# Performance work log

Measured on AMD Instinct MI355X. Metric: run time of the kernel, lower is better.

Reference implementation:

```python
import jax, jax.numpy as jnp
import numpy as np

EMBED_DIM = 128
NUM_HEADS = 4
WIN = (7, 7)
N = WIN[0] * WIN[1]  # 49
NW = 64              # windows per image
B = 128              # batch of images
SCALE = (EMBED_DIM // NUM_HEADS) ** -0.5


def _relative_position_index():
    coords = np.stack(np.meshgrid(np.arange(WIN[0]), np.arange(WIN[1]), indexing='ij'))
    cf = coords.reshape(2, -1)                       # [2, N]
    rel = cf[:, :, None] - cf[:, None, :]            # [2, N, N]
    rel = rel.transpose(1, 2, 0).astype(np.int64)    # [N, N, 2]
    rel[..., 0] += WIN[0] - 1
    rel[..., 0] *= 2 * WIN[1] - 1
    rel[..., 1] += WIN[1] - 1
    return rel.sum(-1).reshape(-1)                   # [N*N]


def setup_inputs() -> dict:
    key = jax.random.key(0)
    ks = jax.random.split(key, 6)
    C = EMBED_DIM
    x = jax.random.normal(ks[0], (NW * B, N, C), dtype=jnp.float32)
    mask = jnp.zeros((NW, N, N), dtype=jnp.float32)
    qkv_w = jax.random.normal(ks[1], (3 * C, C), dtype=jnp.float32) * (C ** -0.5)
    qkv_b = jnp.zeros((3 * C,), dtype=jnp.float32)
    proj_w = jax.random.normal(ks[2], (C, C), dtype=jnp.float32) * (C ** -0.5)
    proj_b = jnp.zeros((C,), dtype=jnp.float32)
    bias_table = jax.random.normal(ks[3], ((2 * WIN[0] - 1) * (2 * WIN[1] - 1), NUM_HEADS), dtype=jnp.float32) * 0.02
    rel_index = jnp.asarray(_relative_position_index(), dtype=jnp.int32)
    return {"x": x, "mask": mask, "qkv_w": qkv_w, "qkv_b": qkv_b,
            "proj_w": proj_w, "proj_b": proj_b, "bias_table": bias_table,
            "rel_index": rel_index}


def reference(x, mask, qkv_w, qkv_b, proj_w, proj_b, bias_table, rel_index):
    nwb, n, c = x.shape
    nh, ch = NUM_HEADS, c // NUM_HEADS
    qkv = x @ qkv_w.T + qkv_b                               # [nwb, n, 3c]
    qkv = qkv.reshape(nwb, n, 3, nh, ch)
    q, k, v = (jnp.moveaxis(qkv, (2, 3), (0, 2))[i] for i in range(3))  # each [nwb, nh, n, ch]
    attn = jnp.einsum('whik,whjk->whij', q * SCALE, k)      # [nwb, nh, n, n]
    # relative position bias: gather then reshape to [1, nh, n, n]
    bias = bias_table[rel_index].reshape(n, n, nh).transpose(2, 0, 1)[None]
    attn = attn + bias
    if mask is not None:
        nw = mask.shape[0]
        attn = attn.reshape(nwb // nw, nw, nh, n, n) + mask[None, :, None]
        attn = attn.reshape(nwb, nh, n, n)
    attn = jax.nn.softmax(attn, axis=-1)
    out = jnp.einsum('whij,whjd->whid', attn, v)            # [nwb, nh, n, ch]
    out = out.transpose(0, 2, 1, 3).reshape(nwb, n, c)
    return out @ proj_w.T + proj_b
```

## Files before the change

kernel.cpp:

```cpp
#include <hip/hip_runtime.h>

typedef __bf16 bf16x8 __attribute__((ext_vector_type(8)));
typedef float  f32x4  __attribute__((ext_vector_type(4)));

#define NTOK  49
#define CDIM  128
#define QK_SCALE 0.17677669529663687f

#define XS 136
#define QS 264
#define VS 72
#define PS 64

#define WQKV_OFF  0
#define WPROJ_OFF 98304
#define BIASF_OFF 131072

__global__ void prep_kernel(const float* __restrict__ qkv_w,
                            const float* __restrict__ proj_w,
                            const float* __restrict__ bias_table,
                            const int*   __restrict__ rel_index,
                            __bf16* __restrict__ wqkv,
                            __bf16* __restrict__ wproj,
                            float*  __restrict__ biasf) {
    int t = blockIdx.x * 256 + threadIdx.x;
    if (t < 384 * 128) wqkv[t]  = (__bf16)qkv_w[t];
    if (t < 128 * 128) wproj[t] = (__bf16)proj_w[t];
    if (t < 4 * 2401) {
        int h = t / 2401, ij = t % 2401;
        biasf[t] = bias_table[rel_index[ij] * 4 + h];
    }
}

__launch_bounds__(256, 2)
__global__ void winattn_kernel(const float* __restrict__ x,
                               const float* __restrict__ mask,
                               const float* __restrict__ qkv_b,
                               const float* __restrict__ proj_b,
                               const __bf16* __restrict__ wqkv,
                               const __bf16* __restrict__ wproj,
                               const float* __restrict__ biasf,
                               float* __restrict__ out) {
    __shared__ __bf16 lds_x[64 * XS];
    __shared__ __bf16 lds_qkv[64 * QS];
    __shared__ __bf16 lds_vt[128 * VS];
    __bf16* lds_p = lds_qkv;

    const int tid  = threadIdx.x;
    const int w    = blockIdx.x;
    const int wave = tid >> 6;
    const int lane = tid & 63;
    const int quad = lane >> 4;
    const int l16  = lane & 15;

    {
        int row = tid >> 2;
        int c0  = (tid & 3) * 32;
        __align__(16) __bf16 tmp[32];
        if (row < NTOK) {
            const float4* src = (const float4*)(x + ((size_t)w * NTOK + row) * CDIM + c0);
            #pragma unroll
            for (int i = 0; i < 8; ++i) {
                float4 f = src[i];
                tmp[i*4+0] = (__bf16)f.x; tmp[i*4+1] = (__bf16)f.y;
                tmp[i*4+2] = (__bf16)f.z; tmp[i*4+3] = (__bf16)f.w;
            }
        } else {
            #pragma unroll
            for (int i = 0; i < 32; ++i) tmp[i] = (__bf16)0.0f;
        }
        bf16x8* dst = (bf16x8*)&lds_x[row * XS + c0];
        #pragma unroll
        for (int i = 0; i < 4; ++i) dst[i] = *(bf16x8*)&tmp[i*8];
    }
    __syncthreads();

    #pragma unroll
    for (int half = 0; half < 2; ++half) {
        f32x4 acc[3][4];
        #pragma unroll
        for (int a = 0; a < 3; ++a)
            #pragma unroll
            for (int b = 0; b < 4; ++b) acc[a][b] = (f32x4){0.f,0.f,0.f,0.f};

        #pragma unroll
        for (int kt = 0; kt < 4; ++kt) {
            bf16x8 a4[4];
            #pragma unroll
            for (int mt = 0; mt < 4; ++mt)
                a4[mt] = *(bf16x8*)&lds_x[(mt*16 + l16) * XS + kt*32 + quad*8];
            #pragma unroll
            for (int ntl = 0; ntl < 3; ++ntl) {
                int o = (wave*6 + half*3 + ntl) * 16 + l16;
                bf16x8 bf = *(const bf16x8*)(wqkv + (size_t)o * CDIM + kt*32 + quad*8);
                #pragma unroll
                for (int mt = 0; mt < 4; ++mt)
                    acc[ntl][mt] = __builtin_amdgcn_mfma_f32_16x16x32_bf16(
                        a4[mt], bf, acc[ntl][mt], 0, 0, 0);
            }
        }
        #pragma unroll
        for (int ntl = 0; ntl < 3; ++ntl) {
            int o = (wave*6 + half*3 + ntl) * 16 + l16;
            float b = qkv_b[o];
            #pragma unroll
            for (int mt = 0; mt < 4; ++mt) {
                #pragma unroll
                for (int r = 0; r < 4; ++r) {
                    int row = mt*16 + quad*4 + r;
                    float v = acc[ntl][mt][r] + b;
                    if (o < 128)       lds_qkv[row * QS + o] = (__bf16)(v * QK_SCALE);
                    else if (o < 256)  lds_qkv[row * QS + o] = (__bf16)v;
                    else               lds_vt[(o - 256) * VS + row] = (__bf16)v;
                }
            }
        }
    }
    __syncthreads();

    {
        const int h = wave;
        bf16x8 bk[4];
        #pragma unroll
        for (int nt = 0; nt < 4; ++nt)
            bk[nt] = *(bf16x8*)&lds_qkv[(nt*16 + l16) * QS + 128 + h*32 + quad*8];

        f32x4 s[4][4];
        #pragma unroll
        for (int mt = 0; mt < 4; ++mt) {
            bf16x8 aq = *(bf16x8*)&lds_qkv[(mt*16 + l16) * QS + h*32 + quad*8];
            #pragma unroll
            for (int nt = 0; nt < 4; ++nt) {
                f32x4 z = (f32x4){0.f,0.f,0.f,0.f};
                s[mt][nt] = __builtin_amdgcn_mfma_f32_16x16x32_bf16(aq, bk[nt], z, 0, 0, 0);
            }
        }

        const float* bh = biasf + h * 2401;
        const float* mh = mask + (size_t)(w & 63) * 2401;
        #pragma unroll
        for (int mt = 0; mt < 4; ++mt) {
            #pragma unroll
            for (int r = 0; r < 4; ++r) {
                int i = mt*16 + quad*4 + r;
                float v[4];
                #pragma unroll
                for (int nt = 0; nt < 4; ++nt) {
                    int j = nt*16 + l16;
                    float t = s[mt][nt][r];
                    if (j < NTOK) { if (i < NTOK) t += bh[i*49 + j] + mh[i*49 + j]; }
                    else t = -1e30f;
                    v[nt] = t;
                }
                float mx = fmaxf(fmaxf(v[0], v[1]), fmaxf(v[2], v[3]));
                mx = fmaxf(mx, __shfl_xor(mx, 1, 64));
                mx = fmaxf(mx, __shfl_xor(mx, 2, 64));
                mx = fmaxf(mx, __shfl_xor(mx, 4, 64));
                mx = fmaxf(mx, __shfl_xor(mx, 8, 64));
                float e[4], sum = 0.f;
                #pragma unroll
                for (int nt = 0; nt < 4; ++nt) { e[nt] = __expf(v[nt] - mx); sum += e[nt]; }
                sum += __shfl_xor(sum, 1, 64);
                sum += __shfl_xor(sum, 2, 64);
                sum += __shfl_xor(sum, 4, 64);
                sum += __shfl_xor(sum, 8, 64);
                float inv = 1.0f / sum;
                #pragma unroll
                for (int nt = 0; nt < 4; ++nt) s[mt][nt][r] = e[nt] * inv;
            }
        }
        __syncthreads();
        #pragma unroll
        for (int mt = 0; mt < 4; ++mt)
            #pragma unroll
            for (int r = 0; r < 4; ++r)
                #pragma unroll
                for (int nt = 0; nt < 4; ++nt)
                    lds_p[((h << 6) + mt*16 + quad*4 + r) * PS + nt*16 + l16] =
                        (__bf16)s[mt][nt][r];
    }
    __syncthreads();

    {
        const int h = wave;
        bf16x8 bv[2][2];
        #pragma unroll
        for (int nv = 0; nv < 2; ++nv)
            #pragma unroll
            for (int kt = 0; kt < 2; ++kt)
                bv[nv][kt] = *(bf16x8*)&lds_vt[(h*32 + nv*16 + l16) * VS + kt*32 + quad*8];

        f32x4 oacc[4][2];
        #pragma unroll
        for (int a = 0; a < 4; ++a)
            #pragma unroll
            for (int b = 0; b < 2; ++b) oacc[a][b] = (f32x4){0.f,0.f,0.f,0.f};

        #pragma unroll
        for (int mt = 0; mt < 4; ++mt)
            #pragma unroll
            for (int kt = 0; kt < 2; ++kt) {
                bf16x8 ap = *(bf16x8*)&lds_p[((h << 6) + mt*16 + l16) * PS + kt*32 + quad*8];
                #pragma unroll
                for (int nv = 0; nv < 2; ++nv)
                    oacc[mt][nv] = __builtin_amdgcn_mfma_f32_16x16x32_bf16(
                        ap, bv[nv][kt], oacc[mt][nv], 0, 0, 0);
            }

        #pragma unroll
        for (int mt = 0; mt < 4; ++mt)
            #pragma unroll
            for (int nv = 0; nv < 2; ++nv)
                #pragma unroll
                for (int r = 0; r < 4; ++r) {
                    int row = mt*16 + quad*4 + r;
                    lds_x[row * XS + h*32 + nv*16 + l16] = (__bf16)oacc[mt][nv][r];
                }
    }
    __syncthreads();

    #pragma unroll
    for (int ntl = 0; ntl < 2; ++ntl) {
        int o = (wave*2 + ntl) * 16 + l16;
        f32x4 acc[4];
        #pragma unroll
        for (int a = 0; a < 4; ++a) acc[a] = (f32x4){0.f,0.f,0.f,0.f};
        #pragma unroll
        for (int kt = 0; kt < 4; ++kt) {
            bf16x8 bf = *(const bf16x8*)(wproj + (size_t)o * CDIM + kt*32 + quad*8);
            #pragma unroll
            for (int mt = 0; mt < 4; ++mt) {
                bf16x8 af = *(bf16x8*)&lds_x[(mt*16 + l16) * XS + kt*32 + quad*8];
                acc[mt] = __builtin_amdgcn_mfma_f32_16x16x32_bf16(af, bf, acc[mt], 0, 0, 0);
            }
        }
        float pb = proj_b[o];
        #pragma unroll
        for (int mt = 0; mt < 4; ++mt)
            #pragma unroll
            for (int r = 0; r < 4; ++r) {
                int row = mt*16 + quad*4 + r;
                if (row < NTOK)
                    out[((size_t)w * NTOK + row) * CDIM + o] = acc[mt][r] + pb;
            }
    }
}

extern "C" void kernel_launch(void* const* d_in, const int* in_sizes, int n_in,
                              void* d_out, int out_size, void* d_ws, size_t ws_size,
                              hipStream_t stream) {
    const float* x          = (const float*)d_in[0];
    const float* mask       = (const float*)d_in[1];
    const float* qkv_w      = (const float*)d_in[2];
    const float* qkv_b      = (const float*)d_in[3];
    const float* proj_w     = (const float*)d_in[4];
    const float* proj_b     = (const float*)d_in[5];
    const float* bias_table = (const float*)d_in[6];
    const int*   rel_index  = (const int*)d_in[7];

    __bf16* wqkv  = (__bf16*)((char*)d_ws + WQKV_OFF);
    __bf16* wproj = (__bf16*)((char*)d_ws + WPROJ_OFF);
    float*  biasf = (float*)((char*)d_ws + BIASF_OFF);

    int nwb = in_sizes[0] / (NTOK * CDIM);

    prep_kernel<<<192, 256, 0, stream>>>(qkv_w, proj_w, bias_table, rel_index,
                                         wqkv, wproj, biasf);
    winattn_kernel<<<nwb, 256, 0, stream>>>(x, mask, qkv_b, proj_b,
                                            wqkv, wproj, biasf, (float*)d_out);
}
```

Measured before the change: 639.6 us.

## Swizzle LDS layout, shrink shared memory, and raise occupancy to three blocks

Replaces the padded LDS buffers with two compact XOR-swizzled buffers, so shared memory per block drops enough to allow three blocks per CU, and launch bounds are raised to match. The QKV projection is reorganised so each wave produces interleaved Q, K and V column tiles. V is held in registers and written transposed into the freed x buffer after the barrier. P and V operands are loaded into registers before an extra barrier so that buffers can be reused. The cost is more index arithmetic per access, an extra barrier, and register pressure from the tighter launch bound.

```diff
diff --git a/kernel.cpp b/kernel.cpp
--- a/kernel.cpp
+++ b/kernel.cpp
@@ -1,20 +1,20 @@
 #include <hip/hip_runtime.h>
 
 typedef __bf16 bf16x8 __attribute__((ext_vector_type(8)));
+typedef __bf16 bf16x4 __attribute__((ext_vector_type(4)));
 typedef float  f32x4  __attribute__((ext_vector_type(4)));
 
 #define NTOK  49
 #define CDIM  128
 #define QK_SCALE 0.17677669529663687f
 
-#define XS 136
-#define QS 264
-#define VS 72
-#define PS 64
-
 #define WQKV_OFF  0
 #define WPROJ_OFF 98304
 #define BIASF_OFF 131072
+
+__device__ __forceinline__ int swz(int row, int col) {
+    return (col & ~63) | ((((col >> 3) ^ row) & 7) << 3) | (col & 7);
+}
 
 __global__ void prep_kernel(const float* __restrict__ qkv_w,
                             const float* __restrict__ proj_w,
@@ -32,7 +32,7 @@
     }
 }
 
-__launch_bounds__(256, 2)
+__launch_bounds__(256, 3)
 __global__ void winattn_kernel(const float* __restrict__ x,
                                const float* __restrict__ mask,
                                const float* __restrict__ qkv_b,
@@ -41,10 +41,8 @@
                                const __bf16* __restrict__ wproj,
                                const float* __restrict__ biasf,
                                float* __restrict__ out) {
-    __shared__ __bf16 lds_x[64 * XS];
-    __shared__ __bf16 lds_qkv[64 * QS];
-    __shared__ __bf16 lds_vt[128 * VS];
-    __bf16* lds_p = lds_qkv;
+    __shared__ __bf16 lds_a[64 * 128];
+    __shared__ __bf16 lds_b[64 * 256];
 
     const int tid  = threadIdx.x;
     const int w    = blockIdx.x;
@@ -69,14 +67,18 @@
             #pragma unroll
             for (int i = 0; i < 32; ++i) tmp[i] = (__bf16)0.0f;
         }
-        bf16x8* dst = (bf16x8*)&lds_x[row * XS + c0];
-        #pragma unroll
-        for (int i = 0; i < 4; ++i) dst[i] = *(bf16x8*)&tmp[i*8];
-    }
-    __syncthreads();
-
+        #pragma unroll
+        for (int i = 0; i < 4; ++i)
+            *(bf16x8*)&lds_a[row * 128 + swz(row, c0 + i*8)] = *(bf16x8*)&tmp[i*8];
+    }
+    __syncthreads();
+
+    bf16x4 vreg[2][4];
     #pragma unroll
     for (int half = 0; half < 2; ++half) {
+        const int oq = (half*4 + wave) * 16 + l16;
+        const int ok = 128 + (wave*2 + half) * 16 + l16;
+        const int ov = 256 + (half*4 + wave) * 16 + l16;
         f32x4 acc[3][4];
         #pragma unroll
         for (int a = 0; a < 3; ++a)
@@ -87,48 +89,60 @@
         for (int kt = 0; kt < 4; ++kt) {
             bf16x8 a4[4];
             #pragma unroll
-            for (int mt = 0; mt < 4; ++mt)
-                a4[mt] = *(bf16x8*)&lds_x[(mt*16 + l16) * XS + kt*32 + quad*8];
-            #pragma unroll
-            for (int ntl = 0; ntl < 3; ++ntl) {
-                int o = (wave*6 + half*3 + ntl) * 16 + l16;
-                bf16x8 bf = *(const bf16x8*)(wqkv + (size_t)o * CDIM + kt*32 + quad*8);
-                #pragma unroll
-                for (int mt = 0; mt < 4; ++mt)
-                    acc[ntl][mt] = __builtin_amdgcn_mfma_f32_16x16x32_bf16(
-                        a4[mt], bf, acc[ntl][mt], 0, 0, 0);
-            }
-        }
-        #pragma unroll
-        for (int ntl = 0; ntl < 3; ++ntl) {
-            int o = (wave*6 + half*3 + ntl) * 16 + l16;
-            float b = qkv_b[o];
-            #pragma unroll
             for (int mt = 0; mt < 4; ++mt) {
-                #pragma unroll
-                for (int r = 0; r < 4; ++r) {
-                    int row = mt*16 + quad*4 + r;
-                    float v = acc[ntl][mt][r] + b;
-                    if (o < 128)       lds_qkv[row * QS + o] = (__bf16)(v * QK_SCALE);
-                    else if (o < 256)  lds_qkv[row * QS + o] = (__bf16)v;
-                    else               lds_vt[(o - 256) * VS + row] = (__bf16)v;
-                }
-            }
-        }
-    }
-    __syncthreads();
+                int rr = mt*16 + l16;
+                a4[mt] = *(bf16x8*)&lds_a[rr * 128 + swz(rr, kt*32 + quad*8)];
+            }
+            bf16x8 bq = *(const bf16x8*)(wqkv + (size_t)oq * CDIM + kt*32 + quad*8);
+            bf16x8 bk = *(const bf16x8*)(wqkv + (size_t)ok * CDIM + kt*32 + quad*8);
+            bf16x8 bv = *(const bf16x8*)(wqkv + (size_t)ov * CDIM + kt*32 + quad*8);
+            #pragma unroll
+            for (int mt = 0; mt < 4; ++mt) {
+                acc[0][mt] = __builtin_amdgcn_mfma_f32_16x16x32_bf16(a4[mt], bq, acc[0][mt], 0, 0, 0);
+                acc[1][mt] = __builtin_amdgcn_mfma_f32_16x16x32_bf16(a4[mt], bk, acc[1][mt], 0, 0, 0);
+                acc[2][mt] = __builtin_amdgcn_mfma_f32_16x16x32_bf16(a4[mt], bv, acc[2][mt], 0, 0, 0);
+            }
+        }
+        float bqb = qkv_b[oq], bkb = qkv_b[ok], bvb = qkv_b[ov];
+        #pragma unroll
+        for (int mt = 0; mt < 4; ++mt) {
+            #pragma unroll
+            for (int r = 0; r < 4; ++r) {
+                int row = mt*16 + quad*4 + r;
+                lds_b[row*256 + swz(row, oq)] = (__bf16)((acc[0][mt][r] + bqb) * QK_SCALE);
+                lds_b[row*256 + swz(row, ok)] = (__bf16)(acc[1][mt][r] + bkb);
+            }
+            bf16x4 vv;
+            #pragma unroll
+            for (int r = 0; r < 4; ++r) vv[r] = (__bf16)(acc[2][mt][r] + bvb);
+            vreg[half][mt] = vv;
+        }
+    }
+    __syncthreads();
+
+    #pragma unroll
+    for (int half = 0; half < 2; ++half) {
+        int vc = (half*4 + wave) * 16 + l16;
+        #pragma unroll
+        for (int mt = 0; mt < 4; ++mt) {
+            int tok = mt*16 + quad*4;
+            *(bf16x4*)&lds_a[vc * 64 + swz(vc, tok)] = vreg[half][mt];
+        }
+    }
 
     {
         const int h = wave;
         bf16x8 bk[4];
         #pragma unroll
-        for (int nt = 0; nt < 4; ++nt)
-            bk[nt] = *(bf16x8*)&lds_qkv[(nt*16 + l16) * QS + 128 + h*32 + quad*8];
-
+        for (int nt = 0; nt < 4; ++nt) {
+            int rr = nt*16 + l16;
+            bk[nt] = *(bf16x8*)&lds_b[rr*256 + swz(rr, 128 + h*32 + quad*8)];
+        }
         f32x4 s[4][4];
         #pragma unroll
         for (int mt = 0; mt < 4; ++mt) {
-            bf16x8 aq = *(bf16x8*)&lds_qkv[(mt*16 + l16) * QS + h*32 + quad*8];
+            int rr = mt*16 + l16;
+            bf16x8 aq = *(bf16x8*)&lds_b[rr*256 + swz(rr, h*32 + quad*8)];
             #pragma unroll
             for (int nt = 0; nt < 4; ++nt) {
                 f32x4 z = (f32x4){0.f,0.f,0.f,0.f};
@@ -173,11 +187,12 @@
         #pragma unroll
         for (int mt = 0; mt < 4; ++mt)
             #pragma unroll
-            for (int r = 0; r < 4; ++r)
+            for (int r = 0; r < 4; ++r) {
+                int prow = (h << 6) + mt*16 + quad*4 + r;
                 #pragma unroll
                 for (int nt = 0; nt < 4; ++nt)
-                    lds_p[((h << 6) + mt*16 + quad*4 + r) * PS + nt*16 + l16] =
-                        (__bf16)s[mt][nt][r];
+                    lds_b[prow*64 + swz(prow, nt*16 + l16)] = (__bf16)s[mt][nt][r];
+            }
     }
     __syncthreads();
 
@@ -187,25 +202,33 @@
         #pragma unroll
         for (int nv = 0; nv < 2; ++nv)
             #pragma unroll
+            for (int kt = 0; kt < 2; ++kt) {
+                int vr = h*32 + nv*16 + l16;
+                bv[nv][kt] = *(bf16x8*)&lds_a[vr*64 + swz(vr, kt*32 + quad*8)];
+            }
+        bf16x8 ap[4][2];
+        #pragma unroll
+        for (int mt = 0; mt < 4; ++mt)
+            #pragma unroll
+            for (int kt = 0; kt < 2; ++kt) {
+                int pr = (h << 6) + mt*16 + l16;
+                ap[mt][kt] = *(bf16x8*)&lds_b[pr*64 + swz(pr, kt*32 + quad*8)];
+            }
+        __syncthreads();
+
+        f32x4 oacc[4][2];
+        #pragma unroll
+        for (int a = 0; a < 4; ++a)
+            #pragma unroll
+            for (int b = 0; b < 2; ++b) oacc[a][b] = (f32x4){0.f,0.f,0.f,0.f};
+        #pragma unroll
+        for (int mt = 0; mt < 4; ++mt)
+            #pragma unroll
             for (int kt = 0; kt < 2; ++kt)
-                bv[nv][kt] = *(bf16x8*)&lds_vt[(h*32 + nv*16 + l16) * VS + kt*32 + quad*8];
-
-        f32x4 oacc[4][2];
-        #pragma unroll
-        for (int a = 0; a < 4; ++a)
-            #pragma unroll
-            for (int b = 0; b < 2; ++b) oacc[a][b] = (f32x4){0.f,0.f,0.f,0.f};
-
-        #pragma unroll
-        for (int mt = 0; mt < 4; ++mt)
-            #pragma unroll
-            for (int kt = 0; kt < 2; ++kt) {
-                bf16x8 ap = *(bf16x8*)&lds_p[((h << 6) + mt*16 + l16) * PS + kt*32 + quad*8];
                 #pragma unroll
                 for (int nv = 0; nv < 2; ++nv)
                     oacc[mt][nv] = __builtin_amdgcn_mfma_f32_16x16x32_bf16(
-                        ap, bv[nv][kt], oacc[mt][nv], 0, 0, 0);
-            }
+                        ap[mt][kt], bv[nv][kt], oacc[mt][nv], 0, 0, 0);
 
         #pragma unroll
         for (int mt = 0; mt < 4; ++mt)
@@ -214,7 +237,7 @@
                 #pragma unroll
                 for (int r = 0; r < 4; ++r) {
                     int row = mt*16 + quad*4 + r;
-                    lds_x[row * XS + h*32 + nv*16 + l16] = (__bf16)oacc[mt][nv][r];
+                    lds_b[row*128 + swz(row, h*32 + nv*16 + l16)] = (__bf16)oacc[mt][nv][r];
                 }
     }
     __syncthreads();
@@ -230,7 +253,8 @@
             bf16x8 bf = *(const bf16x8*)(wproj + (size_t)o * CDIM + kt*32 + quad*8);
             #pragma unroll
             for (int mt = 0; mt < 4; ++mt) {
-                bf16x8 af = *(bf16x8*)&lds_x[(mt*16 + l16) * XS + kt*32 + quad*8];
+                int rr = mt*16 + l16;
+                bf16x8 af = *(bf16x8*)&lds_b[rr*128 + swz(rr, kt*32 + quad*8)];
                 acc[mt] = __builtin_amdgcn_mfma_f32_16x16x32_bf16(af, bf, acc[mt], 0, 0, 0);
             }
         }
```

After: 551.1 us. 13.8% less time.
